# Kernel tuning notes

Measured on AMD Instinct MI355X. Metric: run time of the kernel, lower is better.

The kernel has to match this reference:

```python
import jax, jax.numpy as jnp
import numpy as np

DIM = 384
HEADS = 6
HEAD_DIM = DIM // HEADS
HIDDEN = 4 * DIM
EPS = 1e-5


def layer_norm(x, w, b):
    m = jnp.mean(x, axis=-1, keepdims=True)
    v = jnp.mean((x - m) ** 2, axis=-1, keepdims=True)
    return (x - m) * jax.lax.rsqrt(v + EPS) * w + b


def setup_inputs() -> dict:
    key = jax.random.key(0)
    ks = jax.random.split(key, 8)
    B, N = 2, 4096
    s_in = 1.0 / np.sqrt(DIM)
    s_h = 1.0 / np.sqrt(HIDDEN)
    return {
        "x": jax.random.normal(ks[0], (B, N, DIM), dtype=jnp.float32),
        "qkv_w": jax.random.normal(ks[1], (3 * DIM, DIM), dtype=jnp.float32) * s_in,
        "proj_w": jax.random.normal(ks[2], (DIM, DIM), dtype=jnp.float32) * s_in,
        "proj_b": jnp.zeros((DIM,), dtype=jnp.float32),
        "ln1_w": jnp.ones((DIM,), dtype=jnp.float32),
        "ln1_b": jnp.zeros((DIM,), dtype=jnp.float32),
        "ln2_w": jnp.ones((DIM,), dtype=jnp.float32),
        "ln2_b": jnp.zeros((DIM,), dtype=jnp.float32),
        "fc1_w": jax.random.normal(ks[3], (HIDDEN, DIM), dtype=jnp.float32) * s_in,
        "fc1_b": jnp.zeros((HIDDEN,), dtype=jnp.float32),
        "fc2_w": jax.random.normal(ks[4], (DIM, HIDDEN), dtype=jnp.float32) * s_h,
        "fc2_b": jnp.zeros((DIM,), dtype=jnp.float32),
    }


def reference(x, qkv_w, proj_w, proj_b, ln1_w, ln1_b, ln2_w, ln2_b,
              fc1_w, fc1_b, fc2_w, fc2_b):
    B, N, C = x.shape
    scale = HEAD_DIM ** (-0.5)

    # pre-norm attention
    y = layer_norm(x, ln1_w, ln1_b)
    qkv = (y @ qkv_w.T).reshape(B, N, 3, HEADS, HEAD_DIM)
    qkv = jnp.transpose(qkv, (2, 0, 3, 1, 4))  # [3, B, H, N, D]
    q, k, v = qkv[0], qkv[1], qkv[2]
    attn = jnp.einsum("bhnd,bhmd->bhnm", q, k) * scale  # [B,H,N,N]
    attn = jax.nn.softmax(attn, axis=-1)
    y = jnp.einsum("bhnm,bhmd->bhnd", attn, v)
    y = jnp.transpose(y, (0, 2, 1, 3)).reshape(B, N, C)
    y = y @ proj_w.T + proj_b

    # residual + LN2 + MLP (faithful to source: output = 2 * mlp(ln2(x + y)))
    x = x + y
    x = layer_norm(x, ln2_w, ln2_b)
    h = jax.nn.gelu(x @ fc1_w.T + fc1_b, approximate=False)
    x = h @ fc2_w.T + fc2_b
    x = x + x
    return x
```

## Files before the change

kernel.cpp:

```cpp
#include <hip/hip_runtime.h>
#include <hip/hip_bf16.h>

#define DIM 384
#define HEADS 6
#define HD 64
#define HIDDEN 1536
#define SEQ 4096
#define BATCH 2
#define NTOK (BATCH*SEQ)
#define QKVN (3*DIM)

typedef __attribute__((ext_vector_type(4))) float f32x4;
typedef __attribute__((ext_vector_type(16))) float f32x16;
typedef __attribute__((ext_vector_type(8))) short s16x8;
typedef __attribute__((ext_vector_type(4))) unsigned int u32x4;

__device__ __forceinline__ ushort f2bf(float f) {
    union { float f; unsigned u; } v; v.f = f;
    unsigned r = v.u + 0x7FFF + ((v.u >> 16) & 1);
    return (ushort)(r >> 16);
}
__device__ __forceinline__ float bf2f(ushort b) {
    union { unsigned u; float f; } v; v.u = ((unsigned)b) << 16;
    return v.f;
}
__device__ __forceinline__ unsigned cvtpk(float lo, float hi) {
    unsigned r;
    asm("v_cvt_pk_bf16_f32 %0, %1, %2" : "=v"(r) : "v"(lo), "v"(hi));
    return r;
}
__device__ __forceinline__ void pl32swap(unsigned& a, unsigned& b) {
    asm volatile("v_permlane32_swap_b32 %0, %1" : "+v"(a), "+v"(b));
}
__device__ __forceinline__ void g2l(const ushort* g, ushort* s) {
    __builtin_amdgcn_global_load_lds((const __attribute__((address_space(1))) void*)g,
                                     (__attribute__((address_space(3))) void*)s, 16, 0, 0);
}

__global__ void cvt4_kernel(const float4* __restrict__ s0, ushort* __restrict__ d0, int n0,
                            const float4* __restrict__ s1, ushort* __restrict__ d1, int n1,
                            const float4* __restrict__ s2, ushort* __restrict__ d2, int n2,
                            const float4* __restrict__ s3, ushort* __restrict__ d3, int n3) {
    int i = blockIdx.x * 256 + threadIdx.x;
    const float4* s; ushort* d; int k = i;
    if (i < n0) { s = s0; d = d0; }
    else { k -= n0; if (k < n1) { s = s1; d = d1; }
        else { k -= n1; if (k < n2) { s = s2; d = d2; }
            else { k -= n2; if (k >= n3) return; s = s3; d = d3; } } }
    float4 v = s[k];
    ushort4 o; o.x = f2bf(v.x); o.y = f2bf(v.y); o.z = f2bf(v.z); o.w = f2bf(v.w);
    *(ushort4*)(d + (size_t)k * 4) = o;
}

__global__ __launch_bounds__(256) void ln_kernel(const float* __restrict__ x,
        const float* __restrict__ w, const float* __restrict__ b,
        ushort* __restrict__ y) {
    int l = threadIdx.x & 63;
    int row = blockIdx.x * 4 + (threadIdx.x >> 6);
    const float* xr = x + (size_t)row * DIM;
    float v[6], s = 0.f, s2 = 0.f;
#pragma unroll
    for (int i = 0; i < 6; ++i) { v[i] = xr[l + 64*i]; s += v[i]; s2 += v[i]*v[i]; }
#pragma unroll
    for (int d = 1; d < 64; d <<= 1) { s += __shfl_xor(s, d); s2 += __shfl_xor(s2, d); }
    float mean = s * (1.f/DIM);
    float var  = s2 * (1.f/DIM) - mean*mean;
    float rstd = rsqrtf(var + 1e-5f);
    ushort* yr = y + (size_t)row * DIM;
#pragma unroll
    for (int i = 0; i < 6; ++i) {
        int c = l + 64*i;
        yr[c] = f2bf((v[i]-mean)*rstd*w[c] + b[c]);
    }
}

template<int EPI, int BN>
__global__ __launch_bounds__(256) void gemm_kernel(
        const ushort* __restrict__ A, const ushort* __restrict__ W,
        const float* __restrict__ bias, const float* __restrict__ resid,
        void* __restrict__ Cout, int M, int N, int K) {
    __shared__ __align__(16) ushort lds_a[128*32];
    __shared__ __align__(16) ushort lds_b[BN*32];
    const int t = threadIdx.x, l = t & 63, wid = t >> 6;
    const int lo = l & 15, lg = l >> 4;
    const int m0 = blockIdx.x * 128, n0 = blockIdx.y * BN;
    constexpr int MI = (BN == 128) ? 4 : 2;
    const int wrow = (BN == 128) ? (wid >> 1) * 64 : wid * 32;
    const int wcol = (BN == 128) ? (wid & 1) * 64 : 0;
    f32x4 acc[MI][4] = {};
    const int srow = l >> 2, scol = (l & 3) * 8;
    const ushort* gA0 = A + (size_t)(m0 + wid*16 + srow) * K + scol;
    const ushort* gA1 = A + (size_t)(m0 + (wid+4)*16 + srow) * K + scol;
    const ushort* gB0 = W + (size_t)(n0 + wid*16 + srow) * K + scol;
    const ushort* gB1 = W + (size_t)(n0 + ((wid+4)*16 % BN) + srow) * K + scol;
    ushort* la0 = &lds_a[wid * 512];
    ushort* la1 = &lds_a[(wid + 4) * 512];
    ushort* lb0 = &lds_b[wid * 512];
    ushort* lb1 = (BN == 128) ? &lds_b[(wid + 4) * 512] : nullptr;

    for (int k0 = 0; k0 < K; k0 += 32) {
        g2l(gA0 + k0, la0);
        g2l(gA1 + k0, la1);
        g2l(gB0 + k0, lb0);
        if constexpr (BN == 128) g2l(gB1 + k0, lb1);
        __syncthreads();
        s16x8 af[MI], bf[4];
#pragma unroll
        for (int mi = 0; mi < MI; ++mi)
            af[mi] = *(const s16x8*)&lds_a[(wrow + mi*16 + lo)*32 + lg*8];
#pragma unroll
        for (int ni = 0; ni < 4; ++ni)
            bf[ni] = *(const s16x8*)&lds_b[(wcol + ni*16 + lo)*32 + lg*8];
#pragma unroll
        for (int mi = 0; mi < MI; ++mi)
#pragma unroll
            for (int ni = 0; ni < 4; ++ni)
                acc[mi][ni] = __builtin_amdgcn_mfma_f32_16x16x32_bf16(af[mi], bf[ni], acc[mi][ni], 0,0,0);
        __syncthreads();
    }
#pragma unroll
    for (int mi = 0; mi < MI; ++mi)
#pragma unroll
    for (int ni = 0; ni < 4; ++ni)
#pragma unroll
    for (int r = 0; r < 4; ++r) {
        int row = m0 + wrow + mi*16 + lg*4 + r;
        int col = n0 + wcol + ni*16 + lo;
        float c = acc[mi][ni][r];
        size_t idx = (size_t)row * N + col;
        if (EPI == 0) {
            ((ushort*)Cout)[idx] = f2bf(c);
        } else if (EPI == 1) {
            ((float*)Cout)[idx] = c + bias[col] + resid[idx];
        } else if (EPI == 2) {
            c += bias[col];
            ((ushort*)Cout)[idx] = f2bf(0.5f * c * (1.f + erff(c * 0.70710678118f)));
        } else {
            ((float*)Cout)[idx] = 2.f * (c + bias[col]);
        }
    }
}

#define PV_STEP(S, MM, CB) do {                                                   \
    unsigned w0 = cvtpk(S[8*MM+0], S[8*MM+1]);                                    \
    unsigned w1 = cvtpk(S[8*MM+2], S[8*MM+3]);                                    \
    unsigned w2 = cvtpk(S[8*MM+4], S[8*MM+5]);                                    \
    unsigned w3 = cvtpk(S[8*MM+6], S[8*MM+7]);                                    \
    pl32swap(w0, w2); pl32swap(w1, w3);                                           \
    u32x4 fw = {w0, w1, w2, w3};                                                  \
    s16x8 pa = __builtin_bit_cast(s16x8, fw);                                     \
    int colb = ((CB) + G*8) ^ swz0;                                               \
    s16x8 vb0 = *(const s16x8*)&lds_v[half][q31][colb];                           \
    s16x8 vb1 = *(const s16x8*)&lds_v[half][32 + q31][colb ^ 32];                 \
    o0 = __builtin_amdgcn_mfma_f32_32x32x16_bf16(pa, vb0, o0, 0,0,0);             \
    o1 = __builtin_amdgcn_mfma_f32_32x32x16_bf16(pa, vb1, o1, 0,0,0);             \
} while (0)

__global__ __launch_bounds__(256, 3) void attn_kernel(const ushort* __restrict__ qkv,
                                                      ushort* __restrict__ out) {
    __shared__ __align__(16) ushort lds_k[2][64][72];
    __shared__ __align__(16) ushort lds_v[2][64][72];
    const int t = threadIdx.x, l = t & 63, wid = t >> 6;
    const int G = l >> 5, q31 = l & 31, half = wid >> 1;
    const int b = blockIdx.y / HEADS, h = blockIdx.y % HEADS;
    const ushort* base = qkv + (size_t)b * SEQ * QKVN + h * HD;
    const int q0 = blockIdx.x * 64 + (wid & 1) * 32;

    const float QSC = 0.1803368801111137f;
    s16x8 qf[4];
#pragma unroll
    for (int dc = 0; dc < 4; ++dc) {
        s16x8 qv = *(const s16x8*)(base + (size_t)(q0 + q31) * QKVN + dc*16 + G*8);
#pragma unroll
        for (int j = 0; j < 8; ++j)
            qv[j] = (short)f2bf(bf2f((ushort)qv[j]) * QSC);
        qf[dc] = qv;
    }

    f32x16 o0 = {}, o1 = {};
    float l_run = 0.f;

    const int u = t & 127, sa = u >> 3, sc = u & 7;
    const ushort* kbase = base + DIM;
    const ushort* vbase = base + 2*DIM;
    const int key0base = half * (SEQ/2);
    const int swz0 = ((q31 >> 3) & 3) << 3;

    s16x8 kreg[4];
#pragma unroll
    for (int p = 0; p < 4; ++p)
        kreg[p] = *(const s16x8*)(kbase + (size_t)(key0base + p*16 + sa) * QKVN + sc*8);

    for (int it = 0; it < 32; ++it) {
        const int key0 = key0base + it*64;
        s16x8 vreg[4];
#pragma unroll
        for (int p = 0; p < 4; ++p)
            vreg[p] = *(const s16x8*)(vbase + (size_t)(key0 + p*16 + sa) * QKVN + sc*8);
        __syncthreads();
#pragma unroll
        for (int p = 0; p < 4; ++p) {
            *(s16x8*)&lds_k[half][p*16 + sa][sc*8] = kreg[p];
            const int colp = (p*16 + sa) ^ ((sc & 3) << 3) ^ ((sc >> 2) << 5);
#pragma unroll
            for (int j = 0; j < 8; ++j)
                lds_v[half][sc*8 + j][colp] = (ushort)vreg[p][j];
        }
        __syncthreads();
        if (it < 31) {
#pragma unroll
            for (int p = 0; p < 4; ++p)
                kreg[p] = *(const s16x8*)(kbase + (size_t)(key0 + 64 + p*16 + sa) * QKVN + sc*8);
        }

        f32x16 st0 = {}, st1 = {};
        __builtin_amdgcn_s_setprio(1);
#pragma unroll
        for (int dc = 0; dc < 4; ++dc) {
            s16x8 kf0 = *(const s16x8*)&lds_k[half][q31][dc*16 + G*8];
            s16x8 kf1 = *(const s16x8*)&lds_k[half][32 + q31][dc*16 + G*8];
            st0 = __builtin_amdgcn_mfma_f32_32x32x16_bf16(kf0, qf[dc], st0, 0,0,0);
            st1 = __builtin_amdgcn_mfma_f32_32x32x16_bf16(kf1, qf[dc], st1, 0,0,0);
        }
        __builtin_amdgcn_s_setprio(0);

        float c0 = 0.f, c1 = 0.f, c2 = 0.f, c3 = 0.f;
#pragma unroll
        for (int r = 0; r < 16; r += 4) {
            st0[r]   = exp2f(st0[r]);   c0 += st0[r];
            st0[r+1] = exp2f(st0[r+1]); c1 += st0[r+1];
            st0[r+2] = exp2f(st0[r+2]); c2 += st0[r+2];
            st0[r+3] = exp2f(st0[r+3]); c3 += st0[r+3];
            st1[r]   = exp2f(st1[r]);   c0 += st1[r];
            st1[r+1] = exp2f(st1[r+1]); c1 += st1[r+1];
            st1[r+2] = exp2f(st1[r+2]); c2 += st1[r+2];
            st1[r+3] = exp2f(st1[r+3]); c3 += st1[r+3];
        }
        l_run += (c0 + c1) + (c2 + c3);

        __builtin_amdgcn_s_setprio(1);
        PV_STEP(st0, 0, 0);
        PV_STEP(st0, 1, 16);
        PV_STEP(st1, 0, 32);
        PV_STEP(st1, 1, 48);
        __builtin_amdgcn_s_setprio(0);
    }

    l_run += __shfl_xor(l_run, 32);

    __syncthreads();
    float* mb = (float*)&lds_k[0][0][0];
    float* ml = (float*)&lds_v[0][0][0];
    if (half == 1) {
#pragma unroll
        for (int r = 0; r < 16; ++r) {
            mb[((wid&1)*2 + 0)*1024 + r*64 + l] = o0[r];
            mb[((wid&1)*2 + 1)*1024 + r*64 + l] = o1[r];
        }
        ml[(wid&1)*64 + l] = l_run;
    }
    __syncthreads();
    if (half == 0) {
        float lt = l_run + ml[(wid&1)*64 + l];
        float inv = 1.0f / lt;
        ushort* ob = out + (size_t)b * SEQ * DIM + h * HD;
#pragma unroll
        for (int r = 0; r < 16; ++r) {
            int qr = (r & 3) + 8*(r >> 2) + 4*G;
            float invr = __shfl(inv, qr);
            float v0 = (o0[r] + mb[((wid&1)*2 + 0)*1024 + r*64 + l]) * invr;
            float v1 = (o1[r] + mb[((wid&1)*2 + 1)*1024 + r*64 + l]) * invr;
            int row = q0 + qr;
            ob[(size_t)row * DIM + q31]      = f2bf(v0);
            ob[(size_t)row * DIM + 32 + q31] = f2bf(v1);
        }
    }
}

extern "C" void kernel_launch(void* const* d_in, const int* in_sizes, int n_in,
                              void* d_out, int out_size, void* d_ws, size_t ws_size,
                              hipStream_t stream) {
    const float* x      = (const float*)d_in[0];
    const float* qkv_w  = (const float*)d_in[1];
    const float* proj_w = (const float*)d_in[2];
    const float* proj_b = (const float*)d_in[3];
    const float* ln1_w  = (const float*)d_in[4];
    const float* ln1_b  = (const float*)d_in[5];
    const float* ln2_w  = (const float*)d_in[6];
    const float* ln2_b  = (const float*)d_in[7];
    const float* fc1_w  = (const float*)d_in[8];
    const float* fc1_b  = (const float*)d_in[9];
    const float* fc2_w  = (const float*)d_in[10];
    const float* fc2_b  = (const float*)d_in[11];
    float* outp = (float*)d_out;

    char* ws = (char*)d_ws;
    size_t off = 0;
    auto alloc = [&](size_t bytes) {
        off = (off + 255) & ~(size_t)255;
        void* p = ws + off;
        off += bytes;
        return p;
    };
    ushort* wq   = (ushort*)alloc((size_t)QKVN * DIM * 2);
    ushort* wp   = (ushort*)alloc((size_t)DIM * DIM * 2);
    ushort* w1   = (ushort*)alloc((size_t)HIDDEN * DIM * 2);
    ushort* w2   = (ushort*)alloc((size_t)DIM * HIDDEN * 2);
    ushort* y1   = (ushort*)alloc((size_t)NTOK * DIM * 2);
    ushort* qkvb = (ushort*)alloc((size_t)NTOK * QKVN * 2);
    ushort* ao   = (ushort*)alloc((size_t)NTOK * DIM * 2);
    float*  res  = (float*) alloc((size_t)NTOK * DIM * 4);
    ushort* y2   = (ushort*)alloc((size_t)NTOK * DIM * 2);
    ushort* hb   = (ushort*)alloc((size_t)NTOK * HIDDEN * 2);

    const int n0 = QKVN*DIM/4, n1 = DIM*DIM/4, n2 = HIDDEN*DIM/4, n3 = DIM*HIDDEN/4;
    cvt4_kernel<<<(n0+n1+n2+n3 + 255)/256, 256, 0, stream>>>(
        (const float4*)qkv_w, wq, n0, (const float4*)proj_w, wp, n1,
        (const float4*)fc1_w, w1, n2, (const float4*)fc2_w, w2, n3);

    ln_kernel<<<NTOK/4, 256, 0, stream>>>(x, ln1_w, ln1_b, y1);
    gemm_kernel<0,128><<<dim3(NTOK/128, QKVN/128), 256, 0, stream>>>(y1, wq, nullptr, nullptr, qkvb, NTOK, QKVN, DIM);
    attn_kernel<<<dim3(SEQ/64, BATCH*HEADS), 256, 0, stream>>>(qkvb, ao);
    gemm_kernel<1,64><<<dim3(NTOK/128, DIM/64), 256, 0, stream>>>(ao, wp, proj_b, x, res, NTOK, DIM, DIM);
    ln_kernel<<<NTOK/4, 256, 0, stream>>>(res, ln2_w, ln2_b, y2);
    gemm_kernel<2,128><<<dim3(NTOK/128, HIDDEN/128), 256, 0, stream>>>(y2, w1, fc1_b, nullptr, hb, NTOK, HIDDEN, DIM);
    gemm_kernel<3,64><<<dim3(NTOK/128, DIM/64), 256, 0, stream>>>(hb, w2, fc2_b, nullptr, outp, NTOK, DIM, HIDDEN);
}
```

Before: 270.3 us.

## Retile GEMMs to 64-row blocks with swizzled K64 LDS, compute softmax denominator via MFMA

The GEMM kernel now uses 64-row M tiles with a 64-wide K step, an XOR-swizzled LDS layout to avoid bank conflicts, and a launch-bounds occupancy hint. The launch grids are doubled in M to match. The attention kernel drops the scalar row-sum reduction and instead accumulates the softmax denominator with an extra MFMA against a vector of ones. It also prefetches V one iteration ahead alongside K. These changes aim to raise GEMM occupancy and overlap, and to remove VALU work in attention. The cost is extra MFMA work and more registers from the added accumulator and V prefetch.

```diff
diff --git a/kernel.cpp b/kernel.cpp
--- a/kernel.cpp
+++ b/kernel.cpp
@@ -75,57 +75,71 @@
 }
 
 template<int EPI, int BN>
-__global__ __launch_bounds__(256) void gemm_kernel(
+__global__ __launch_bounds__(256, 4) void gemm_kernel(
         const ushort* __restrict__ A, const ushort* __restrict__ W,
         const float* __restrict__ bias, const float* __restrict__ resid,
         void* __restrict__ Cout, int M, int N, int K) {
-    __shared__ __align__(16) ushort lds_a[128*32];
-    __shared__ __align__(16) ushort lds_b[BN*32];
+    __shared__ __align__(16) ushort lds_a[64*64];
+    __shared__ __align__(16) ushort lds_w[BN*64];
     const int t = threadIdx.x, l = t & 63, wid = t >> 6;
     const int lo = l & 15, lg = l >> 4;
-    const int m0 = blockIdx.x * 128, n0 = blockIdx.y * BN;
-    constexpr int MI = (BN == 128) ? 4 : 2;
-    const int wrow = (BN == 128) ? (wid >> 1) * 64 : wid * 32;
-    const int wcol = (BN == 128) ? (wid & 1) * 64 : 0;
-    f32x4 acc[MI][4] = {};
-    const int srow = l >> 2, scol = (l & 3) * 8;
-    const ushort* gA0 = A + (size_t)(m0 + wid*16 + srow) * K + scol;
-    const ushort* gA1 = A + (size_t)(m0 + (wid+4)*16 + srow) * K + scol;
-    const ushort* gB0 = W + (size_t)(n0 + wid*16 + srow) * K + scol;
-    const ushort* gB1 = W + (size_t)(n0 + ((wid+4)*16 % BN) + srow) * K + scol;
-    ushort* la0 = &lds_a[wid * 512];
-    ushort* la1 = &lds_a[(wid + 4) * 512];
-    ushort* lb0 = &lds_b[wid * 512];
-    ushort* lb1 = (BN == 128) ? &lds_b[(wid + 4) * 512] : nullptr;
-
-    for (int k0 = 0; k0 < K; k0 += 32) {
-        g2l(gA0 + k0, la0);
-        g2l(gA1 + k0, la1);
-        g2l(gB0 + k0, lb0);
-        if constexpr (BN == 128) g2l(gB1 + k0, lb1);
+    const int m0 = blockIdx.x * 64, n0 = blockIdx.y * BN;
+    constexpr int NI = BN / 32;
+    constexpr int WW = BN / 32;
+    const int wm = (wid & 1) * 32, wn = (wid >> 1) * (BN / 2);
+    f32x4 acc[2][NI] = {};
+
+    const int srow8 = l >> 3;
+    const int schunk = (l & 7) ^ srow8;
+    const ushort* gA[2];
+    ushort* lA[2];
+#pragma unroll
+    for (int w = 0; w < 2; ++w) {
+        gA[w] = A + (size_t)(m0 + wid*16 + w*8 + srow8) * K + schunk*8;
+        lA[w] = &lds_a[(wid*16 + w*8)*64];
+    }
+    const ushort* gW[WW];
+    ushort* lW[WW];
+#pragma unroll
+    for (int w = 0; w < WW; ++w) {
+        gW[w] = W + (size_t)(n0 + wid*(8*WW) + w*8 + srow8) * K + schunk*8;
+        lW[w] = &lds_w[(wid*(8*WW) + w*8)*64];
+    }
+
+    const int lo7 = lo & 7;
+    for (int k0 = 0; k0 < K; k0 += 64) {
+        if (k0) __syncthreads();
+#pragma unroll
+        for (int w = 0; w < 2; ++w)  g2l(gA[w] + k0, lA[w]);
+#pragma unroll
+        for (int w = 0; w < WW; ++w) g2l(gW[w] + k0, lW[w]);
         __syncthreads();
-        s16x8 af[MI], bf[4];
-#pragma unroll
-        for (int mi = 0; mi < MI; ++mi)
-            af[mi] = *(const s16x8*)&lds_a[(wrow + mi*16 + lo)*32 + lg*8];
-#pragma unroll
-        for (int ni = 0; ni < 4; ++ni)
-            bf[ni] = *(const s16x8*)&lds_b[(wcol + ni*16 + lo)*32 + lg*8];
-#pragma unroll
-        for (int mi = 0; mi < MI; ++mi)
-#pragma unroll
-            for (int ni = 0; ni < 4; ++ni)
-                acc[mi][ni] = __builtin_amdgcn_mfma_f32_16x16x32_bf16(af[mi], bf[ni], acc[mi][ni], 0,0,0);
-        __syncthreads();
-    }
-#pragma unroll
-    for (int mi = 0; mi < MI; ++mi)
-#pragma unroll
-    for (int ni = 0; ni < 4; ++ni)
+#pragma unroll
+        for (int kk = 0; kk < 2; ++kk) {
+            const int ch = ((kk*4 + lg) ^ lo7) * 8;
+            s16x8 af[2], bfr[NI];
+#pragma unroll
+            for (int mi = 0; mi < 2; ++mi)
+                af[mi] = *(const s16x8*)&lds_a[(wm + mi*16 + lo)*64 + ch];
+#pragma unroll
+            for (int ni = 0; ni < NI; ++ni)
+                bfr[ni] = *(const s16x8*)&lds_w[(wn + ni*16 + lo)*64 + ch];
+#pragma unroll
+            for (int mi = 0; mi < 2; ++mi)
+#pragma unroll
+                for (int ni = 0; ni < NI; ++ni)
+                    acc[mi][ni] = __builtin_amdgcn_mfma_f32_16x16x32_bf16(af[mi], bfr[ni], acc[mi][ni], 0,0,0);
+        }
+    }
+
+#pragma unroll
+    for (int mi = 0; mi < 2; ++mi)
+#pragma unroll
+    for (int ni = 0; ni < NI; ++ni)
 #pragma unroll
     for (int r = 0; r < 4; ++r) {
-        int row = m0 + wrow + mi*16 + lg*4 + r;
-        int col = n0 + wcol + ni*16 + lo;
+        int row = m0 + wm + mi*16 + lg*4 + r;
+        int col = n0 + wn + ni*16 + lo;
         float c = acc[mi][ni][r];
         size_t idx = (size_t)row * N + col;
         if (EPI == 0) {
@@ -154,6 +168,7 @@
     s16x8 vb1 = *(const s16x8*)&lds_v[half][32 + q31][colb ^ 32];                 \
     o0 = __builtin_amdgcn_mfma_f32_32x32x16_bf16(pa, vb0, o0, 0,0,0);             \
     o1 = __builtin_amdgcn_mfma_f32_32x32x16_bf16(pa, vb1, o1, 0,0,0);             \
+    ol = __builtin_amdgcn_mfma_f32_32x32x16_bf16(pa, vones, ol, 0,0,0);           \
 } while (0)
 
 __global__ __launch_bounds__(256, 3) void attn_kernel(const ushort* __restrict__ qkv,
@@ -176,9 +191,11 @@
             qv[j] = (short)f2bf(bf2f((ushort)qv[j]) * QSC);
         qf[dc] = qv;
     }
-
-    f32x16 o0 = {}, o1 = {};
-    float l_run = 0.f;
+    s16x8 vones;
+#pragma unroll
+    for (int j = 0; j < 8; ++j) vones[j] = (short)0x3F80;
+
+    f32x16 o0 = {}, o1 = {}, ol = {};
 
     const int u = t & 127, sa = u >> 3, sc = u & 7;
     const ushort* kbase = base + DIM;
@@ -186,17 +203,15 @@
     const int key0base = half * (SEQ/2);
     const int swz0 = ((q31 >> 3) & 3) << 3;
 
-    s16x8 kreg[4];
-#pragma unroll
-    for (int p = 0; p < 4; ++p)
+    s16x8 kreg[4], vreg[4];
+#pragma unroll
+    for (int p = 0; p < 4; ++p) {
         kreg[p] = *(const s16x8*)(kbase + (size_t)(key0base + p*16 + sa) * QKVN + sc*8);
+        vreg[p] = *(const s16x8*)(vbase + (size_t)(key0base + p*16 + sa) * QKVN + sc*8);
+    }
 
     for (int it = 0; it < 32; ++it) {
         const int key0 = key0base + it*64;
-        s16x8 vreg[4];
-#pragma unroll
-        for (int p = 0; p < 4; ++p)
-            vreg[p] = *(const s16x8*)(vbase + (size_t)(key0 + p*16 + sa) * QKVN + sc*8);
         __syncthreads();
 #pragma unroll
         for (int p = 0; p < 4; ++p) {
@@ -209,8 +224,10 @@
         __syncthreads();
         if (it < 31) {
 #pragma unroll
-            for (int p = 0; p < 4; ++p)
+            for (int p = 0; p < 4; ++p) {
                 kreg[p] = *(const s16x8*)(kbase + (size_t)(key0 + 64 + p*16 + sa) * QKVN + sc*8);
+                vreg[p] = *(const s16x8*)(vbase + (size_t)(key0 + 64 + p*16 + sa) * QKVN + sc*8);
+            }
         }
 
         f32x16 st0 = {}, st1 = {};
@@ -224,19 +241,11 @@
         }
         __builtin_amdgcn_s_setprio(0);
 
-        float c0 = 0.f, c1 = 0.f, c2 = 0.f, c3 = 0.f;
-#pragma unroll
-        for (int r = 0; r < 16; r += 4) {
-            st0[r]   = exp2f(st0[r]);   c0 += st0[r];
-            st0[r+1] = exp2f(st0[r+1]); c1 += st0[r+1];
-            st0[r+2] = exp2f(st0[r+2]); c2 += st0[r+2];
-            st0[r+3] = exp2f(st0[r+3]); c3 += st0[r+3];
-            st1[r]   = exp2f(st1[r]);   c0 += st1[r];
-            st1[r+1] = exp2f(st1[r+1]); c1 += st1[r+1];
-            st1[r+2] = exp2f(st1[r+2]); c2 += st1[r+2];
-            st1[r+3] = exp2f(st1[r+3]); c3 += st1[r+3];
-        }
-        l_run += (c0 + c1) + (c2 + c3);
+#pragma unroll
+        for (int r = 0; r < 16; ++r) {
+            st0[r] = exp2f(st0[r]);
+            st1[r] = exp2f(st1[r]);
+        }
 
         __builtin_amdgcn_s_setprio(1);
         PV_STEP(st0, 0, 0);
@@ -246,8 +255,6 @@
         __builtin_amdgcn_s_setprio(0);
     }
 
-    l_run += __shfl_xor(l_run, 32);
-
     __syncthreads();
     float* mb = (float*)&lds_k[0][0][0];
     float* ml = (float*)&lds_v[0][0][0];
@@ -256,20 +263,18 @@
         for (int r = 0; r < 16; ++r) {
             mb[((wid&1)*2 + 0)*1024 + r*64 + l] = o0[r];
             mb[((wid&1)*2 + 1)*1024 + r*64 + l] = o1[r];
-        }
-        ml[(wid&1)*64 + l] = l_run;
+            ml[(wid&1)*1024 + r*64 + l] = ol[r];
+        }
     }
     __syncthreads();
     if (half == 0) {
-        float lt = l_run + ml[(wid&1)*64 + l];
-        float inv = 1.0f / lt;
         ushort* ob = out + (size_t)b * SEQ * DIM + h * HD;
 #pragma unroll
         for (int r = 0; r < 16; ++r) {
-            int qr = (r & 3) + 8*(r >> 2) + 4*G;
-            float invr = __shfl(inv, qr);
+            float invr = 1.0f / (ol[r] + ml[(wid&1)*1024 + r*64 + l]);
             float v0 = (o0[r] + mb[((wid&1)*2 + 0)*1024 + r*64 + l]) * invr;
             float v1 = (o1[r] + mb[((wid&1)*2 + 1)*1024 + r*64 + l]) * invr;
+            int qr = (r & 3) + 8*(r >> 2) + 4*G;
             int row = q0 + qr;
             ob[(size_t)row * DIM + q31]      = f2bf(v0);
             ob[(size_t)row * DIM + 32 + q31] = f2bf(v1);
@@ -319,10 +324,10 @@
         (const float4*)fc1_w, w1, n2, (const float4*)fc2_w, w2, n3);
 
     ln_kernel<<<NTOK/4, 256, 0, stream>>>(x, ln1_w, ln1_b, y1);
-    gemm_kernel<0,128><<<dim3(NTOK/128, QKVN/128), 256, 0, stream>>>(y1, wq, nullptr, nullptr, qkvb, NTOK, QKVN, DIM);
+    gemm_kernel<0,128><<<dim3(NTOK/64, QKVN/128), 256, 0, stream>>>(y1, wq, nullptr, nullptr, qkvb, NTOK, QKVN, DIM);
     attn_kernel<<<dim3(SEQ/64, BATCH*HEADS), 256, 0, stream>>>(qkvb, ao);
-    gemm_kernel<1,64><<<dim3(NTOK/128, DIM/64), 256, 0, stream>>>(ao, wp, proj_b, x, res, NTOK, DIM, DIM);
+    gemm_kernel<1,64><<<dim3(NTOK/64, DIM/64), 256, 0, stream>>>(ao, wp, proj_b, x, res, NTOK, DIM, DIM);
     ln_kernel<<<NTOK/4, 256, 0, stream>>>(res, ln2_w, ln2_b, y2);
-    gemm_kernel<2,128><<<dim3(NTOK/128, HIDDEN/128), 256, 0, stream>>>(y2, w1, fc1_b, nullptr, hb, NTOK, HIDDEN, DIM);
-    gemm_kernel<3,64><<<dim3(NTOK/128, DIM/64), 256, 0, stream>>>(hb, w2, fc2_b, nullptr, outp, NTOK, DIM, HIDDEN);
-}
+    gemm_kernel<2,128><<<dim3(NTOK/64, HIDDEN/128), 256, 0, stream>>>(y2, w1, fc1_b, nullptr, hb, NTOK, HIDDEN, DIM);
+    gemm_kernel<3,64><<<dim3(NTOK/64, DIM/64), 256, 0, stream>>>(hb, w2, fc2_b, nullptr, outp, NTOK, DIM, HIDDEN);
+}
```

After: 248.3 us. 8.1% less time.
